# Performance work log

Hardware: AMD Instinct MI355X
Metric: run time of the kernel (lower is better)

The kernel has to match this reference:

```python
import jax, jax.numpy as jnp
from jax import lax
import numpy as np

K_IN, K_OUT, K_STATE = 64, 64, 256
T_PRE, T_FWD, BATCH = 64, 80, 4096


def setup_inputs() -> dict:
    key = jax.random.key(0)
    ks = jax.random.split(key, 13)
    s = 0.05  # param scale for numerical stability of the recurrences
    return {
        "pre_x": jax.random.normal(ks[0], (T_PRE, BATCH, K_IN), jnp.float32),
        "pre_y": jax.random.normal(ks[1], (T_PRE, BATCH, K_OUT), jnp.float32),
        "forward_x": jax.random.normal(ks[2], (T_FWD, BATCH, K_IN), jnp.float32),
        "A_w": jax.random.normal(ks[3], (K_STATE, K_STATE), jnp.float32) * s,
        "A_b": jax.random.normal(ks[4], (K_STATE,), jnp.float32) * s,
        "B_w": jax.random.normal(ks[5], (K_STATE, K_IN), jnp.float32) * s,
        "B_b": jax.random.normal(ks[6], (K_STATE,), jnp.float32) * s,
        "C_w": jax.random.normal(ks[7], (K_OUT, K_STATE), jnp.float32) * s,
        "C_b": jax.random.normal(ks[8], (K_OUT,), jnp.float32) * s,
        "W_ih": jax.random.normal(ks[9], (K_STATE, K_IN + K_OUT), jnp.float32) * s,
        "b_ih": jax.random.normal(ks[10], (K_STATE,), jnp.float32) * s,
        "W_hh": jax.random.normal(ks[11], (K_STATE, K_STATE), jnp.float32) * s,
        "b_hh": jax.random.normal(ks[12], (K_STATE,), jnp.float32) * s,
    }


def reference(pre_x, pre_y, forward_x, A_w, A_b, B_w, B_b, C_w, C_b,
              W_ih, b_ih, W_hh, b_hh):
    # --- encoder: single-layer tanh RNN over concat(pre_x, pre_y), h0 = 0 ---
    xy = jnp.concatenate([pre_x, pre_y], axis=2)          # [T_pre, B, k_in+k_out]
    # precompute input projection for all steps (one big GEMM)
    inp_proj = xy @ W_ih.T + b_ih                          # [T_pre, B, k_state]

    def rnn_step(h, u):
        h = jnp.tanh(u + h @ W_hh.T + b_hh)
        return h, None

    h0 = jnp.zeros((pre_x.shape[1], W_hh.shape[0]), pre_x.dtype)
    hn, _ = lax.scan(rnn_step, h0, inp_proj)               # hn: [B, k_state]

    # --- state-space rollout: h_t = A h_{t-1} + B x_t ; y_t = C h_t ---
    Bx = forward_x @ B_w.T + (A_b + B_b)                   # fold both biases once

    def ss_step(h, bx):
        h = h @ A_w.T + bx
        return h, h

    _, hs = lax.scan(ss_step, hn, Bx)                      # [T_fwd, B, k_state]
    return hs @ C_w.T + C_b                                # [T_fwd, B, k_out]
```

## Files before the change

kernel.cpp:

```cpp
#include <hip/hip_runtime.h>
#include <hip/hip_bf16.h>

typedef __attribute__((ext_vector_type(8))) short short8;
typedef __attribute__((ext_vector_type(4))) float f32x4;

#define T_PRE 64
#define T_FWD 80
#define BATCHN 4096

#define HP 264
#define IP 136

#define U_WRNN 0
#define U_WSS  98304
#define U_C    180224
#define U_END  196608
#define PREP_N 197120

__device__ __forceinline__ unsigned short bf1(float a) {
  unsigned ua = __float_as_uint(a);
  return (unsigned short)((ua + 0x7fffu + ((ua >> 16) & 1u)) >> 16);
}
__device__ __forceinline__ unsigned pk(float a, float b) {
  __hip_bfloat162 h = __float22bfloat162_rn(make_float2(a, b));
  unsigned u;
  __builtin_memcpy(&u, &h, 4);
  return u;
}
__device__ __forceinline__ float tanh_fast(float x) {
  float e = __expf(2.0f * x);
  return 1.0f - 2.0f * __builtin_amdgcn_rcpf(e + 1.0f);
}

__global__ void prep_kernel(const float* __restrict__ A_w, const float* __restrict__ A_b,
                            const float* __restrict__ B_w, const float* __restrict__ B_b,
                            const float* __restrict__ C_w,
                            const float* __restrict__ W_ih, const float* __restrict__ b_ih,
                            const float* __restrict__ W_hh, const float* __restrict__ b_hh,
                            unsigned short* __restrict__ ws) {
  int i = blockIdx.x * 256 + threadIdx.x;
  if (i < U_WSS) {
    int j = i / 384, k = i - j * 384;
    float v = (k < 256) ? W_hh[j * 256 + k] : W_ih[j * 128 + (k - 256)];
    ws[i] = bf1(v);
  } else if (i < U_C) {
    int ii = i - U_WSS;
    int j = ii / 320, k = ii - j * 320;
    float v = (k < 256) ? A_w[j * 256 + k] : B_w[j * 64 + (k - 256)];
    ws[i] = bf1(v);
  } else if (i < U_END) {
    int ii = i - U_C;
    int o = ii >> 8, k = ii & 255;
    ws[i] = bf1(C_w[o * 256 + k]);
  } else if (i < PREP_N) {
    float* fb = (float*)(ws + U_END);
    int j = i - U_END;
    fb[j] = (j < 256) ? (b_ih[j] + b_hh[j]) : (A_b[j - 256] + B_b[j - 256]);
  }
}

__global__ __launch_bounds__(512, 1) void rnn_ss_kernel(
    const float* __restrict__ pre_x, const float* __restrict__ pre_y,
    const float* __restrict__ fwd_x, const float* __restrict__ C_b,
    const unsigned short* __restrict__ ws, float* __restrict__ out) {
  __shared__ unsigned short hbuf[2][16 * HP];
  __shared__ unsigned short ibuf[2][16 * IP];

  const int tid = threadIdx.x;
  const int lane = tid & 63;
  const int w = tid >> 6;
  const int col = lane & 15;
  const int q = lane >> 4;
  const int r0 = blockIdx.x * 16;
  const int srow = (tid & 255) >> 4;
  const int sc4 = tid & 15;
  const bool xhalf = (tid >= 256);

#pragma unroll
  for (int it = 0; it < 2; ++it) {
    int i = tid + it * 512;
    int r = i >> 6, c = (i & 63) * 4;
    *(uint2*)&hbuf[0][r * HP + c] = make_uint2(0u, 0u);
  }

  const float* fbias = (const float*)(ws + U_END);
  int cur = 0;

  {
    short8 wf[2][12];
#pragma unroll
    for (int mt = 0; mt < 2; ++mt)
#pragma unroll
      for (int kf = 0; kf < 12; ++kf)
        wf[mt][kf] = *(const short8*)(ws + U_WRNN +
                       (size_t)(w * 32 + mt * 16 + col) * 384 + kf * 32 + q * 8);
    f32x4 br[2];
#pragma unroll
    for (int mt = 0; mt < 2; ++mt)
      br[mt] = *(const f32x4*)(fbias + w * 32 + mt * 16 + q * 4);

    {
      f32x4 v = xhalf ? *(const f32x4*)(pre_x + (size_t)(r0 + srow) * 64 + sc4 * 4)
                      : *(const f32x4*)(pre_y + (size_t)(r0 + srow) * 64 + sc4 * 4);
      *(uint2*)&ibuf[0][srow * IP + (xhalf ? 0 : 64) + sc4 * 4] =
          make_uint2(pk(v[0], v[1]), pk(v[2], v[3]));
    }

    for (int t = 0; t < T_PRE; ++t) {
      __syncthreads();
      f32x4 nv;
      bool do_stage = true;
      if (t < T_PRE - 1) {
        nv = xhalf ? *(const f32x4*)(pre_x + ((size_t)(t + 1) * BATCHN + r0 + srow) * 64 + sc4 * 4)
                   : *(const f32x4*)(pre_y + ((size_t)(t + 1) * BATCHN + r0 + srow) * 64 + sc4 * 4);
      } else if (xhalf) {
        nv = *(const f32x4*)(fwd_x + (size_t)(r0 + srow) * 64 + sc4 * 4);
      } else {
        do_stage = false;
      }
      const unsigned short* hc = hbuf[cur];
      const unsigned short* ic = ibuf[cur];
      short8 bfr[12];
#pragma unroll
      for (int kf = 0; kf < 8; ++kf)
        bfr[kf] = *(const short8*)&hc[col * HP + kf * 32 + q * 8];
#pragma unroll
      for (int kf = 8; kf < 12; ++kf)
        bfr[kf] = *(const short8*)&ic[col * IP + (kf - 8) * 32 + q * 8];
      f32x4 acc[2];
#pragma unroll
      for (int mt = 0; mt < 2; ++mt) acc[mt] = br[mt];
#pragma unroll
      for (int kf = 0; kf < 12; ++kf)
#pragma unroll
        for (int mt = 0; mt < 2; ++mt)
          acc[mt] = __builtin_amdgcn_mfma_f32_16x16x32_bf16(wf[mt][kf], bfr[kf], acc[mt], 0, 0, 0);
      unsigned short* hn_ = hbuf[cur ^ 1];
#pragma unroll
      for (int mt = 0; mt < 2; ++mt) {
        float t0 = tanh_fast(acc[mt][0]), t1 = tanh_fast(acc[mt][1]);
        float t2 = tanh_fast(acc[mt][2]), t3 = tanh_fast(acc[mt][3]);
        *(uint2*)&hn_[col * HP + w * 32 + mt * 16 + q * 4] =
            make_uint2(pk(t0, t1), pk(t2, t3));
      }
      if (do_stage)
        *(uint2*)&ibuf[cur ^ 1][srow * IP + (xhalf ? 0 : 64) + sc4 * 4] =
            make_uint2(pk(nv[0], nv[1]), pk(nv[2], nv[3]));
      cur ^= 1;
    }
  }

  {
    short8 sf[2][10];
#pragma unroll
    for (int mt = 0; mt < 2; ++mt)
#pragma unroll
      for (int kf = 0; kf < 10; ++kf)
        sf[mt][kf] = *(const short8*)(ws + U_WSS +
                       (size_t)(w * 32 + mt * 16 + col) * 320 + kf * 32 + q * 8);
    f32x4 bs[2];
#pragma unroll
    for (int mt = 0; mt < 2; ++mt)
      bs[mt] = *(const f32x4*)(fbias + 256 + w * 32 + mt * 16 + q * 4);
    short8 cf[8];
    f32x4 cb;
    if (w < 4) {
#pragma unroll
      for (int kf = 0; kf < 8; ++kf)
        cf[kf] = *(const short8*)(ws + U_C + (size_t)(w * 16 + col) * 256 + kf * 32 + q * 8);
      cb = *(const f32x4*)(C_b + w * 16 + q * 4);
    }

    for (int i = 0; i < T_FWD; ++i) {
      __syncthreads();
      f32x4 nv;
      if (i < T_FWD - 1 && xhalf)
        nv = *(const f32x4*)(fwd_x + ((size_t)(i + 1) * BATCHN + r0 + srow) * 64 + sc4 * 4);
      const unsigned short* hc = hbuf[cur];
      const unsigned short* ic = ibuf[cur];
      short8 bfr[10];
#pragma unroll
      for (int kf = 0; kf < 8; ++kf)
        bfr[kf] = *(const short8*)&hc[col * HP + kf * 32 + q * 8];
#pragma unroll
      for (int kf = 8; kf < 10; ++kf)
        bfr[kf] = *(const short8*)&ic[col * IP + (kf - 8) * 32 + q * 8];
      f32x4 acc[2];
#pragma unroll
      for (int mt = 0; mt < 2; ++mt) acc[mt] = bs[mt];
#pragma unroll
      for (int kf = 0; kf < 10; ++kf)
#pragma unroll
        for (int mt = 0; mt < 2; ++mt)
          acc[mt] = __builtin_amdgcn_mfma_f32_16x16x32_bf16(sf[mt][kf], bfr[kf], acc[mt], 0, 0, 0);
      if (w < 4 && i >= 1) {
        f32x4 y = cb;
#pragma unroll
        for (int kf = 0; kf < 8; ++kf)
          y = __builtin_amdgcn_mfma_f32_16x16x32_bf16(cf[kf], bfr[kf], y, 0, 0, 0);
        *(f32x4*)(out + ((size_t)(i - 1) * BATCHN + r0 + col) * 64 + w * 16 + q * 4) = y;
      }
      unsigned short* hn_ = hbuf[cur ^ 1];
#pragma unroll
      for (int mt = 0; mt < 2; ++mt)
        *(uint2*)&hn_[col * HP + w * 32 + mt * 16 + q * 4] =
            make_uint2(pk(acc[mt][0], acc[mt][1]), pk(acc[mt][2], acc[mt][3]));
      if (i < T_FWD - 1 && xhalf)
        *(uint2*)&ibuf[cur ^ 1][srow * IP + sc4 * 4] =
            make_uint2(pk(nv[0], nv[1]), pk(nv[2], nv[3]));
      cur ^= 1;
    }

    __syncthreads();
    if (w < 4) {
      const unsigned short* hc = hbuf[cur];
      short8 bfr[8];
#pragma unroll
      for (int kf = 0; kf < 8; ++kf)
        bfr[kf] = *(const short8*)&hc[col * HP + kf * 32 + q * 8];
      f32x4 y = cb;
#pragma unroll
      for (int kf = 0; kf < 8; ++kf)
        y = __builtin_amdgcn_mfma_f32_16x16x32_bf16(cf[kf], bfr[kf], y, 0, 0, 0);
      *(f32x4*)(out + ((size_t)(T_FWD - 1) * BATCHN + r0 + col) * 64 + w * 16 + q * 4) = y;
    }
  }
}

extern "C" void kernel_launch(void* const* d_in, const int* in_sizes, int n_in,
                              void* d_out, int out_size, void* d_ws, size_t ws_size,
                              hipStream_t stream) {
  const float* pre_x = (const float*)d_in[0];
  const float* pre_y = (const float*)d_in[1];
  const float* fwd_x = (const float*)d_in[2];
  const float* A_w   = (const float*)d_in[3];
  const float* A_b   = (const float*)d_in[4];
  const float* B_w   = (const float*)d_in[5];
  const float* B_b   = (const float*)d_in[6];
  const float* C_w   = (const float*)d_in[7];
  const float* C_b   = (const float*)d_in[8];
  const float* W_ih  = (const float*)d_in[9];
  const float* b_ih  = (const float*)d_in[10];
  const float* W_hh  = (const float*)d_in[11];
  const float* b_hh  = (const float*)d_in[12];
  unsigned short* ws = (unsigned short*)d_ws;
  float* out = (float*)d_out;

  prep_kernel<<<(PREP_N + 255) / 256, 256, 0, stream>>>(
      A_w, A_b, B_w, B_b, C_w, W_ih, b_ih, W_hh, b_hh, ws);
  rnn_ss_kernel<<<BATCHN / 16, 512, 0, stream>>>(pre_x, pre_y, fwd_x, C_b, ws, out);
}
```

Measured before the change: 323.2 us.

## Advance state-space recurrence two steps per iteration using precomputed A^2 and CA products

```diff
diff --git a/kernel.cpp b/kernel.cpp
--- a/kernel.cpp
+++ b/kernel.cpp
@@ -12,10 +12,12 @@
 #define IP 136
 
 #define U_WRNN 0
-#define U_WSS  98304
-#define U_C    180224
-#define U_END  196608
-#define PREP_N 197120
+#define U_WREC 98304
+#define U_YW   196608
+#define U_FB   245760
+#define U_CAF  247040
+#define PREP1_N 213504
+#define PREP2_N 49280
 
 __device__ __forceinline__ unsigned short bf1(float a) {
   unsigned ua = __float_as_uint(a);
@@ -32,36 +34,109 @@
   return 1.0f - 2.0f * __builtin_amdgcn_rcpf(e + 1.0f);
 }
 
-__global__ void prep_kernel(const float* __restrict__ A_w, const float* __restrict__ A_b,
-                            const float* __restrict__ B_w, const float* __restrict__ B_b,
-                            const float* __restrict__ C_w,
-                            const float* __restrict__ W_ih, const float* __restrict__ b_ih,
-                            const float* __restrict__ W_hh, const float* __restrict__ b_hh,
-                            unsigned short* __restrict__ ws) {
+__global__ void prep1_kernel(const float* __restrict__ A_w, const float* __restrict__ A_b,
+                             const float* __restrict__ B_w, const float* __restrict__ B_b,
+                             const float* __restrict__ W_ih, const float* __restrict__ b_ih,
+                             const float* __restrict__ W_hh, const float* __restrict__ b_hh,
+                             const float* __restrict__ C_w,
+                             unsigned short* __restrict__ ws) {
   int i = blockIdx.x * 256 + threadIdx.x;
-  if (i < U_WSS) {
+  float* fb = (float*)(ws + U_FB);
+  float* caf = (float*)(ws + U_CAF);
+  if (i < 98304) {
     int j = i / 384, k = i - j * 384;
     float v = (k < 256) ? W_hh[j * 256 + k] : W_ih[j * 128 + (k - 256)];
-    ws[i] = bf1(v);
-  } else if (i < U_C) {
-    int ii = i - U_WSS;
-    int j = ii / 320, k = ii - j * 320;
-    float v = (k < 256) ? A_w[j * 256 + k] : B_w[j * 64 + (k - 256)];
-    ws[i] = bf1(v);
-  } else if (i < U_END) {
-    int ii = i - U_C;
-    int o = ii >> 8, k = ii & 255;
-    ws[i] = bf1(C_w[o * 256 + k]);
-  } else if (i < PREP_N) {
-    float* fb = (float*)(ws + U_END);
-    int j = i - U_END;
-    fb[j] = (j < 256) ? (b_ih[j] + b_hh[j]) : (A_b[j - 256] + B_b[j - 256]);
+    ws[U_WRNN + i] = bf1(v);
+  } else if (i < 98560) {
+    int j = i - 98304;
+    fb[j] = b_ih[j] + b_hh[j];
+  } else if (i < 114944) {
+    int ii = i - 98560;
+    int o = ii >> 8, j = ii & 255;
+    float s = 0.f;
+    for (int k = 0; k < 256; ++k) s += C_w[o * 256 + k] * A_w[k * 256 + j];
+    caf[ii] = s;
+  } else if (i < 213248) {
+    int ii = i - 114944;
+    int j = ii / 384, k = ii - j * 384;
+    float v;
+    if (k < 256) {
+      float s = 0.f;
+      for (int kk = 0; kk < 256; ++kk) s += A_w[j * 256 + kk] * A_w[kk * 256 + k];
+      v = s;
+    } else if (k < 320) {
+      int k2 = k - 256;
+      float s = 0.f;
+      for (int kk = 0; kk < 256; ++kk) s += A_w[j * 256 + kk] * B_w[kk * 64 + k2];
+      v = s;
+    } else {
+      v = B_w[j * 64 + (k - 320)];
+    }
+    ws[U_WREC + ii] = bf1(v);
+  } else if (i < PREP1_N) {
+    int j = i - 213248;
+    float s = A_b[j] + B_b[j];
+    for (int k = 0; k < 256; ++k) s += A_w[j * 256 + k] * (A_b[k] + B_b[k]);
+    fb[256 + j] = s;
+  }
+}
+
+__global__ void prep2_kernel(const float* __restrict__ A_w, const float* __restrict__ A_b,
+                             const float* __restrict__ B_w, const float* __restrict__ B_b,
+                             const float* __restrict__ C_w, const float* __restrict__ C_b,
+                             unsigned short* __restrict__ ws) {
+  int i = blockIdx.x * 256 + threadIdx.x;
+  float* fb = (float*)(ws + U_FB);
+  const float* caf = (const float*)(ws + U_CAF);
+  if (i < 24576) {
+    int o = i / 384, k = i - o * 384;
+    float v = 0.f;
+    if (k < 256) {
+      v = caf[o * 256 + k];
+    } else if (k < 320) {
+      int k2 = k - 256;
+      float s = 0.f;
+      for (int kk = 0; kk < 256; ++kk) s += C_w[o * 256 + kk] * B_w[kk * 64 + k2];
+      v = s;
+    }
+    ws[U_YW + i] = bf1(v);
+  } else if (i < 49152) {
+    int ii = i - 24576;
+    int o = ii / 384, k = ii - o * 384;
+    float v;
+    if (k < 256) {
+      float s = 0.f;
+      for (int kk = 0; kk < 256; ++kk) s += caf[o * 256 + kk] * A_w[kk * 256 + k];
+      v = s;
+    } else if (k < 320) {
+      int k2 = k - 256;
+      float s = 0.f;
+      for (int kk = 0; kk < 256; ++kk) s += caf[o * 256 + kk] * B_w[kk * 64 + k2];
+      v = s;
+    } else {
+      int k2 = k - 320;
+      float s = 0.f;
+      for (int kk = 0; kk < 256; ++kk) s += C_w[o * 256 + kk] * B_w[kk * 64 + k2];
+      v = s;
+    }
+    ws[U_YW + 24576 + ii] = bf1(v);
+  } else if (i < PREP2_N) {
+    int ii = i - 49152;
+    int o = ii & 63, which = ii >> 6;
+    float s = C_b[o];
+    if (which == 0) {
+      for (int k = 0; k < 256; ++k) s += C_w[o * 256 + k] * (A_b[k] + B_b[k]);
+    } else {
+      for (int k = 0; k < 256; ++k)
+        s += (caf[o * 256 + k] + C_w[o * 256 + k]) * (A_b[k] + B_b[k]);
+    }
+    fb[512 + which * 64 + o] = s;
   }
 }
 
 __global__ __launch_bounds__(512, 1) void rnn_ss_kernel(
     const float* __restrict__ pre_x, const float* __restrict__ pre_y,
-    const float* __restrict__ fwd_x, const float* __restrict__ C_b,
+    const float* __restrict__ fwd_x,
     const unsigned short* __restrict__ ws, float* __restrict__ out) {
   __shared__ unsigned short hbuf[2][16 * HP];
   __shared__ unsigned short ibuf[2][16 * IP];
@@ -83,7 +158,7 @@
     *(uint2*)&hbuf[0][r * HP + c] = make_uint2(0u, 0u);
   }
 
-  const float* fbias = (const float*)(ws + U_END);
+  const float* fbias = (const float*)(ws + U_FB);
   int cur = 0;
 
   {
@@ -107,17 +182,15 @@
     }
 
     for (int t = 0; t < T_PRE; ++t) {
-      __syncthreads();
       f32x4 nv;
-      bool do_stage = true;
       if (t < T_PRE - 1) {
         nv = xhalf ? *(const f32x4*)(pre_x + ((size_t)(t + 1) * BATCHN + r0 + srow) * 64 + sc4 * 4)
                    : *(const f32x4*)(pre_y + ((size_t)(t + 1) * BATCHN + r0 + srow) * 64 + sc4 * 4);
-      } else if (xhalf) {
-        nv = *(const f32x4*)(fwd_x + (size_t)(r0 + srow) * 64 + sc4 * 4);
       } else {
-        do_stage = false;
+        nv = xhalf ? *(const f32x4*)(fwd_x + (size_t)(r0 + srow) * 64 + sc4 * 4)
+                   : *(const f32x4*)(fwd_x + ((size_t)BATCHN + r0 + srow) * 64 + sc4 * 4);
       }
+      __syncthreads();
       const unsigned short* hc = hbuf[cur];
       const unsigned short* ic = ibuf[cur];
       short8 bfr[12];
@@ -143,86 +216,70 @@
         *(uint2*)&hn_[col * HP + w * 32 + mt * 16 + q * 4] =
             make_uint2(pk(t0, t1), pk(t2, t3));
       }
-      if (do_stage)
+      *(uint2*)&ibuf[cur ^ 1][srow * IP + (xhalf ? 0 : 64) + sc4 * 4] =
+          make_uint2(pk(nv[0], nv[1]), pk(nv[2], nv[3]));
+      cur ^= 1;
+    }
+  }
+
+  {
+    short8 rf[2][12];
+#pragma unroll
+    for (int mt = 0; mt < 2; ++mt)
+#pragma unroll
+      for (int kf = 0; kf < 12; ++kf)
+        rf[mt][kf] = *(const short8*)(ws + U_WREC +
+                       (size_t)(w * 32 + mt * 16 + col) * 384 + kf * 32 + q * 8);
+    f32x4 brv[2];
+#pragma unroll
+    for (int mt = 0; mt < 2; ++mt)
+      brv[mt] = *(const f32x4*)(fbias + 256 + w * 32 + mt * 16 + q * 4);
+
+    const int yi = w >> 2;
+    const int yc = w & 3;
+    short8 yf[12];
+#pragma unroll
+    for (int kf = 0; kf < 12; ++kf)
+      yf[kf] = *(const short8*)(ws + U_YW +
+                 (size_t)(yi * 64 + yc * 16 + col) * 384 + kf * 32 + q * 8);
+    f32x4 ybv = *(const f32x4*)(fbias + 512 + yi * 64 + yc * 16 + q * 4);
+
+    for (int b = 0; b < T_FWD / 2; ++b) {
+      f32x4 nv;
+      const bool st = (b < T_FWD / 2 - 1);
+      if (st)
+        nv = *(const f32x4*)(fwd_x +
+              ((size_t)(2 * b + 2 + (xhalf ? 0 : 1)) * BATCHN + r0 + srow) * 64 + sc4 * 4);
+      __syncthreads();
+      const unsigned short* hc = hbuf[cur];
+      const unsigned short* ic = ibuf[cur];
+      short8 bfr[12];
+#pragma unroll
+      for (int kf = 0; kf < 8; ++kf)
+        bfr[kf] = *(const short8*)&hc[col * HP + kf * 32 + q * 8];
+#pragma unroll
+      for (int kf = 8; kf < 12; ++kf)
+        bfr[kf] = *(const short8*)&ic[col * IP + (kf - 8) * 32 + q * 8];
+      f32x4 acc[2];
+#pragma unroll
+      for (int mt = 0; mt < 2; ++mt) acc[mt] = brv[mt];
+      f32x4 yacc = ybv;
+#pragma unroll
+      for (int kf = 0; kf < 12; ++kf) {
+        acc[0] = __builtin_amdgcn_mfma_f32_16x16x32_bf16(rf[0][kf], bfr[kf], acc[0], 0, 0, 0);
+        acc[1] = __builtin_amdgcn_mfma_f32_16x16x32_bf16(rf[1][kf], bfr[kf], acc[1], 0, 0, 0);
+        yacc   = __builtin_amdgcn_mfma_f32_16x16x32_bf16(yf[kf],    bfr[kf], yacc,   0, 0, 0);
+      }
+      *(f32x4*)(out + ((size_t)(2 * b + yi) * BATCHN + r0 + col) * 64 + yc * 16 + q * 4) = yacc;
+      unsigned short* hn_ = hbuf[cur ^ 1];
+#pragma unroll
+      for (int mt = 0; mt < 2; ++mt)
+        *(uint2*)&hn_[col * HP + w * 32 + mt * 16 + q * 4] =
+            make_uint2(pk(acc[mt][0], acc[mt][1]), pk(acc[mt][2], acc[mt][3]));
+      if (st)
         *(uint2*)&ibuf[cur ^ 1][srow * IP + (xhalf ? 0 : 64) + sc4 * 4] =
             make_uint2(pk(nv[0], nv[1]), pk(nv[2], nv[3]));
       cur ^= 1;
-    }
-  }
-
-  {
-    short8 sf[2][10];
-#pragma unroll
-    for (int mt = 0; mt < 2; ++mt)
-#pragma unroll
-      for (int kf = 0; kf < 10; ++kf)
-        sf[mt][kf] = *(const short8*)(ws + U_WSS +
-                       (size_t)(w * 32 + mt * 16 + col) * 320 + kf * 32 + q * 8);
-    f32x4 bs[2];
-#pragma unroll
-    for (int mt = 0; mt < 2; ++mt)
-      bs[mt] = *(const f32x4*)(fbias + 256 + w * 32 + mt * 16 + q * 4);
-    short8 cf[8];
-    f32x4 cb;
-    if (w < 4) {
-#pragma unroll
-      for (int kf = 0; kf < 8; ++kf)
-        cf[kf] = *(const short8*)(ws + U_C + (size_t)(w * 16 + col) * 256 + kf * 32 + q * 8);
-      cb = *(const f32x4*)(C_b + w * 16 + q * 4);
-    }
-
-    for (int i = 0; i < T_FWD; ++i) {
-      __syncthreads();
-      f32x4 nv;
-      if (i < T_FWD - 1 && xhalf)
-        nv = *(const f32x4*)(fwd_x + ((size_t)(i + 1) * BATCHN + r0 + srow) * 64 + sc4 * 4);
-      const unsigned short* hc = hbuf[cur];
-      const unsigned short* ic = ibuf[cur];
-      short8 bfr[10];
-#pragma unroll
-      for (int kf = 0; kf < 8; ++kf)
-        bfr[kf] = *(const short8*)&hc[col * HP + kf * 32 + q * 8];
-#pragma unroll
-      for (int kf = 8; kf < 10; ++kf)
-        bfr[kf] = *(const short8*)&ic[col * IP + (kf - 8) * 32 + q * 8];
-      f32x4 acc[2];
-#pragma unroll
-      for (int mt = 0; mt < 2; ++mt) acc[mt] = bs[mt];
-#pragma unroll
-      for (int kf = 0; kf < 10; ++kf)
-#pragma unroll
-        for (int mt = 0; mt < 2; ++mt)
-          acc[mt] = __builtin_amdgcn_mfma_f32_16x16x32_bf16(sf[mt][kf], bfr[kf], acc[mt], 0, 0, 0);
-      if (w < 4 && i >= 1) {
-        f32x4 y = cb;
-#pragma unroll
-        for (int kf = 0; kf < 8; ++kf)
-          y = __builtin_amdgcn_mfma_f32_16x16x32_bf16(cf[kf], bfr[kf], y, 0, 0, 0);
-        *(f32x4*)(out + ((size_t)(i - 1) * BATCHN + r0 + col) * 64 + w * 16 + q * 4) = y;
-      }
-      unsigned short* hn_ = hbuf[cur ^ 1];
-#pragma unroll
-      for (int mt = 0; mt < 2; ++mt)
-        *(uint2*)&hn_[col * HP + w * 32 + mt * 16 + q * 4] =
-            make_uint2(pk(acc[mt][0], acc[mt][1]), pk(acc[mt][2], acc[mt][3]));
-      if (i < T_FWD - 1 && xhalf)
-        *(uint2*)&ibuf[cur ^ 1][srow * IP + sc4 * 4] =
-            make_uint2(pk(nv[0], nv[1]), pk(nv[2], nv[3]));
-      cur ^= 1;
-    }
-
-    __syncthreads();
-    if (w < 4) {
-      const unsigned short* hc = hbuf[cur];
-      short8 bfr[8];
-#pragma unroll
-      for (int kf = 0; kf < 8; ++kf)
-        bfr[kf] = *(const short8*)&hc[col * HP + kf * 32 + q * 8];
-      f32x4 y = cb;
-#pragma unroll
-      for (int kf = 0; kf < 8; ++kf)
-        y = __builtin_amdgcn_mfma_f32_16x16x32_bf16(cf[kf], bfr[kf], y, 0, 0, 0);
-      *(f32x4*)(out + ((size_t)(T_FWD - 1) * BATCHN + r0 + col) * 64 + w * 16 + q * 4) = y;
     }
   }
 }
@@ -246,7 +303,9 @@
   unsigned short* ws = (unsigned short*)d_ws;
   float* out = (float*)d_out;
 
-  prep_kernel<<<(PREP_N + 255) / 256, 256, 0, stream>>>(
-      A_w, A_b, B_w, B_b, C_w, W_ih, b_ih, W_hh, b_hh, ws);
-  rnn_ss_kernel<<<BATCHN / 16, 512, 0, stream>>>(pre_x, pre_y, fwd_x, C_b, ws, out);
-}
+  prep1_kernel<<<(PREP1_N + 255) / 256, 256, 0, stream>>>(
+      A_w, A_b, B_w, B_b, W_ih, b_ih, W_hh, b_hh, C_w, ws);
+  prep2_kernel<<<(PREP2_N + 255) / 256, 256, 0, stream>>>(
+      A_w, A_b, B_w, B_b, C_w, C_b, ws);
+  rnn_ss_kernel<<<BATCHN / 16, 512, 0, stream>>>(pre_x, pre_y, fwd_x, ws, out);
+}
```

Result: faster. 304.8 us (-5.7%).
